# Kernel optimization log

Measured on AMD Instinct MI355X. Metric: run time of the kernel, lower is better.

Reference implementation:

```python
import jax, jax.numpy as jnp
import numpy as np

# 8 skeleton directions (unit step vectors (dy, dx)) at 45-degree increments.
# step idx selects the direction along which the 1D kernel taps are sampled.
DIRS = [(0, 1), (1, 1), (1, 0), (1, -1), (0, -1), (-1, -1), (-1, 0), (-1, 1)]
DILATION = 1


def setup_inputs() -> dict:
    key = jax.random.key(0)
    k1, k2 = jax.random.split(key)
    B, C, H, W = 16, 128, 112, 112
    O, K = 128, 3
    x = jax.random.normal(k1, (B, C, H, W), dtype=jnp.float32)
    # kaiming_uniform-like scale for relu: bound = sqrt(6 / fan_in), fan_in = C*K
    bound = float(np.sqrt(6.0 / (C * K)))
    weight = jax.random.uniform(k2, (O, C, K), dtype=jnp.float32, minval=-bound, maxval=bound)
    return {"x": x, "weight": weight}


def _skeleton_conv_all_dirs(x, weight, dilation):
    """Directional 1D conv with zero 'same' padding for each of 8 directions.

    x: [B,C,H,W], weight: [O,C,K] -> out: [B,O,8,H,W]
    out[b,o,d,h,w] = sum_{c,k} w[o,c,k] * x[b,c, h+(k-K//2)*dil*dy_d, w+(k-K//2)*dil*dx_d]
    (out-of-bounds samples treated as zero)
    """
    B, C, H, W = x.shape
    O, _, K = weight.shape
    center = K // 2
    pad = center * dilation
    xp = jnp.pad(x, ((0, 0), (0, 0), (pad, pad), (pad, pad)))
    outs = []
    for dy, dx in DIRS:
        # gather the K taps along this direction: [K, B, C, H, W]
        taps = jnp.stack(
            [
                xp[
                    :,
                    :,
                    pad + (k - center) * dilation * dy : pad + (k - center) * dilation * dy + H,
                    pad + (k - center) * dilation * dx : pad + (k - center) * dilation * dx + W,
                ]
                for k in range(K)
            ],
            axis=0,
        )
        outs.append(jnp.einsum("kbchw,ock->bohw", taps, weight))
    return jnp.stack(outs, axis=2)  # [B, O, 8, H, W]


def reference(x, weight):
    # norm=None, activation=None -> raw stacked directional conv outputs
    return _skeleton_conv_all_dirs(x, weight, DILATION)
```

## Files before the change

kernel.cpp:

```cpp
#include <hip/hip_runtime.h>


#define Bn 16
#define Cn 128
#define On 128
#define Hn 112
#define Wn 112
#define HW 12544
#define PBLK 128
#define LDP 130

typedef short short8 __attribute__((ext_vector_type(8)));
typedef float floatx4 __attribute__((ext_vector_type(4)));

__device__ __forceinline__ unsigned short f2bf(float f) {
    unsigned u = __float_as_uint(f);
    u += 0x7FFFu + ((u >> 16) & 1u);
    return (unsigned short)(u >> 16);
}
__device__ __forceinline__ float bf2f(unsigned short h) {
    return __uint_as_float(((unsigned)h) << 16);
}

__global__ __launch_bounds__(256) void prep_w(const float* __restrict__ w,
                                              unsigned short* __restrict__ wb) {
    int i = blockIdx.x * 256 + threadIdx.x;
    int k = i >> 14;
    int r = i & 16383;
    int o = r >> 7, c = r & 127;
    wb[i] = f2bf(w[(o * Cn + c) * 3 + k]);
}

__global__ __launch_bounds__(256) void k1_gemm(const float* __restrict__ x,
                                               const unsigned short* __restrict__ wb,
                                               unsigned short* __restrict__ yws,
                                               int b0, int yB) {
    __shared__ unsigned short xs[Cn * LDP];
    const int t = threadIdx.x;
    const int wv = t >> 6, lane = t & 63;
    const int n16 = lane & 15, q = lane >> 4;
    const int bl = blockIdx.y;
    const int b = b0 + bl;
    const int pb = blockIdx.x * PBLK;

    {
        const float4* xg = (const float4*)x;
        size_t xbase = (size_t)(b * Cn) * (HW / 4) + (size_t)blockIdx.x * (PBLK / 4);
        #pragma unroll
        for (int i = 0; i < 16; ++i) {
            int idx = i * 256 + t;
            int c = idx >> 5, p4 = (idx & 31) * 4;
            float4 v = xg[xbase + (size_t)c * (HW / 4) + (idx & 31)];
            int la = c * LDP + p4;
            xs[la + 0] = f2bf(v.x); xs[la + 1] = f2bf(v.y);
            xs[la + 2] = f2bf(v.z); xs[la + 3] = f2bf(v.w);
        }
    }

    short8 af[3][2][4];
    #pragma unroll
    for (int kk = 0; kk < 3; ++kk)
        #pragma unroll
        for (int oi = 0; oi < 2; ++oi) {
            int o = wv * 32 + oi * 16 + n16;
            #pragma unroll
            for (int kc = 0; kc < 4; ++kc)
                af[kk][oi][kc] = *(const short8*)(wb + ((kk * On + o) * Cn + kc * 32 + q * 8));
        }
    __syncthreads();

    for (int nt = 0; nt < PBLK / 16; ++nt) {
        int p0 = nt * 16;
        short8 bf[4];
        #pragma unroll
        for (int kc = 0; kc < 4; ++kc) {
            int cb = kc * 32 + q * 8;
            short8 v;
            #pragma unroll
            for (int j = 0; j < 8; ++j) v[j] = (short)xs[(cb + j) * LDP + p0 + n16];
            bf[kc] = v;
        }
        #pragma unroll
        for (int kk = 0; kk < 3; ++kk)
            #pragma unroll
            for (int oi = 0; oi < 2; ++oi) {
                floatx4 acc = {0.f, 0.f, 0.f, 0.f};
                #pragma unroll
                for (int kc = 0; kc < 4; ++kc)
                    acc = __builtin_amdgcn_mfma_f32_16x16x32_bf16(af[kk][oi][kc], bf[kc], acc, 0, 0, 0);
                #pragma unroll
                for (int r = 0; r < 4; ++r) {
                    int orow = wv * 32 + oi * 16 + q * 4 + r;
                    yws[((size_t)(kk * yB + bl) * On + orow) * HW + pb + p0 + n16] = f2bf(acc[r]);
                }
            }
    }
}

#define LROW 128
__global__ __launch_bounds__(448) void k2_combine(const unsigned short* __restrict__ yws,
                                                  float* __restrict__ out,
                                                  int b0, int yB) {
    __shared__ unsigned short yt[3 * 34 * LROW];
    const int t = threadIdx.x;
    const int ht = blockIdx.x;
    const int o = blockIdx.y;
    const int bl = blockIdx.z;
    const int b = b0 + bl;
    const int h0 = ht * 32;

    for (int i = t; i < 3 * 34 * 15; i += 448) {
        int rj = i / 15, seg = i - rj * 15;
        int k = rj / 34, hr = rj - k * 34;
        int h = h0 - 1 + hr;
        if (seg < 14) {
            short8 v = {0, 0, 0, 0, 0, 0, 0, 0};
            if (h >= 0 && h < Hn)
                v = *(const short8*)(yws + ((size_t)(k * yB + bl) * On + o) * HW + h * Wn + seg * 8);
            *(short8*)(yt + (k * 34 + hr) * LROW + 8 + seg * 8) = v;
        } else {
            yt[(k * 34 + hr) * LROW + 7] = 0;
            yt[(k * 34 + hr) * LROW + 120] = 0;
        }
    }
    __syncthreads();

    int hr = t / 14, g = t - hr * 14;
    int h = h0 + hr;
    if (h >= Hn) return;
    int lr = hr + 1;
    int jb = 8 + g * 8;

    float y0[3][10], y2[3][10], y1[8];
    #pragma unroll
    for (int r = 0; r < 3; ++r)
        #pragma unroll
        for (int j = 0; j < 10; ++j) {
            y0[r][j] = bf2f(yt[(0 * 34 + lr - 1 + r) * LROW + jb - 1 + j]);
            y2[r][j] = bf2f(yt[(2 * 34 + lr - 1 + r) * LROW + jb - 1 + j]);
        }
    #pragma unroll
    for (int j = 0; j < 8; ++j) y1[j] = bf2f(yt[(1 * 34 + lr) * LROW + jb + j]);

    const int DY[8] = {0, 1, 1, 1, 0, -1, -1, -1};
    const int DX[8] = {1, 1, 0, -1, -1, -1, 0, 1};
    size_t obase = ((size_t)(b * On + o) * 8) * HW + (size_t)h * Wn + g * 8;
    #pragma unroll
    for (int d = 0; d < 8; ++d) {
        int dy = DY[d], dx = DX[d];
        float vv[8];
        #pragma unroll
        for (int i = 0; i < 8; ++i)
            vv[i] = y1[i] + y0[1 - dy][i + 1 - dx] + y2[1 + dy][i + 1 + dx];
        float4* po = (float4*)(out + obase + (size_t)d * HW);
        po[0] = make_float4(vv[0], vv[1], vv[2], vv[3]);
        po[1] = make_float4(vv[4], vv[5], vv[6], vv[7]);
    }
}

__global__ __launch_bounds__(256) void k_naive(const float* __restrict__ x,
                                               const float* __restrict__ w,
                                               float* __restrict__ out) {
    const int DY[8] = {0, 1, 1, 1, 0, -1, -1, -1};
    const int DX[8] = {1, 1, 0, -1, -1, -1, 0, 1};
    size_t idx = (size_t)blockIdx.x * 256 + threadIdx.x;
    if (idx >= (size_t)Bn * On * 8 * HW) return;
    int ww = idx % Wn; size_t r = idx / Wn;
    int hh = r % Hn; r /= Hn;
    int d = r % 8; r /= 8;
    int o = r % On; int b = (int)(r / On);
    float s = 0.f;
    for (int c = 0; c < Cn; ++c)
        for (int k = 0; k < 3; ++k) {
            int h2 = hh + (k - 1) * DY[d], w2 = ww + (k - 1) * DX[d];
            if (h2 >= 0 && h2 < Hn && w2 >= 0 && w2 < Wn)
                s += w[(o * Cn + c) * 3 + k] * x[(size_t)(b * Cn + c) * HW + h2 * Wn + w2];
        }
    out[idx] = s;
}

extern "C" void kernel_launch(void* const* d_in, const int* in_sizes, int n_in,
                              void* d_out, int out_size, void* d_ws, size_t ws_size,
                              hipStream_t stream) {
    const float* x = (const float*)d_in[0];
    const float* w = (const float*)d_in[1];
    float* out = (float*)d_out;

    unsigned short* wb = (unsigned short*)d_ws;
    unsigned short* yws = (unsigned short*)((char*)d_ws + 98304);
    const size_t perB = (size_t)3 * On * HW * 2;
    size_t avail = ws_size > 98304 ? ws_size - 98304 : 0;
    int nb = (int)(avail / perB);
    if (nb > Bn) nb = Bn;

    if (nb < 1) {
        size_t total = (size_t)Bn * On * 8 * HW;
        k_naive<<<dim3((unsigned)((total + 255) / 256)), 256, 0, stream>>>(x, w, out);
        return;
    }

    prep_w<<<192, 256, 0, stream>>>(w, wb);
    for (int b0 = 0; b0 < Bn; b0 += nb) {
        int cnb = (Bn - b0 < nb) ? (Bn - b0) : nb;
        k1_gemm<<<dim3(HW / PBLK, cnb), 256, 0, stream>>>(x, wb, yws, b0, nb);
        k2_combine<<<dim3(4, On, cnb), 448, 0, stream>>>(yws, out, b0, nb);
    }
}
```

Before: 1.083 ms.

## Fuse GEMM and directional combine into one kernel computing all eight directions

Replaces the two-kernel pipeline, which wrote three per-tap bf16 intermediates to workspace and recombined them, with one kernel. Each block loads a halo tile of x into XOR-swizzled LDS and runs the MFMAs for each direction's shifted taps directly, pairing opposite directions so they share loaded fragments. Removes the intermediate round-trip through global memory and the second launch. In exchange it does more MFMA work, since the per-direction side taps are recomputed instead of shared, and it writes fp32 output as scattered scalar stores.

```diff
diff --git a/kernel.cpp b/kernel.cpp
--- a/kernel.cpp
+++ b/kernel.cpp
@@ -7,8 +7,9 @@
 #define Hn 112
 #define Wn 112
 #define HW 12544
-#define PBLK 128
-#define LDP 130
+
+#define NR 66
+#define LROW 128
 
 typedef short short8 __attribute__((ext_vector_type(8)));
 typedef float floatx4 __attribute__((ext_vector_type(4)));
@@ -17,9 +18,6 @@
     unsigned u = __float_as_uint(f);
     u += 0x7FFFu + ((u >> 16) & 1u);
     return (unsigned short)(u >> 16);
-}
-__device__ __forceinline__ float bf2f(unsigned short h) {
-    return __uint_as_float(((unsigned)h) << 16);
 }
 
 __global__ __launch_bounds__(256) void prep_w(const float* __restrict__ w,
@@ -31,130 +29,116 @@
     wb[i] = f2bf(w[(o * Cn + c) * 3 + k]);
 }
 
-__global__ __launch_bounds__(256) void k1_gemm(const float* __restrict__ x,
-                                               const unsigned short* __restrict__ wb,
-                                               unsigned short* __restrict__ yws,
-                                               int b0, int yB) {
-    __shared__ unsigned short xs[Cn * LDP];
+__global__ __launch_bounds__(256, 2) void conv8(const float* __restrict__ x,
+                                                const unsigned short* __restrict__ wb,
+                                                float* __restrict__ out) {
+    __shared__ unsigned short xs[4 * NR * LROW];
     const int t = threadIdx.x;
     const int wv = t >> 6, lane = t & 63;
     const int n16 = lane & 15, q = lane >> 4;
-    const int bl = blockIdx.y;
-    const int b = b0 + bl;
-    const int pb = blockIdx.x * PBLK;
+    const int bx = blockIdx.x;
+    const int b = blockIdx.y;
+    const int wc = bx & 1, hs = bx >> 1;
+    const int h0 = hs * 2;
+    const int wbase = wc * 64;
+    const int NT = wc ? 3 : 4;
 
     {
-        const float4* xg = (const float4*)x;
-        size_t xbase = (size_t)(b * Cn) * (HW / 4) + (size_t)blockIdx.x * (PBLK / 4);
-        #pragma unroll
-        for (int i = 0; i < 16; ++i) {
-            int idx = i * 256 + t;
-            int c = idx >> 5, p4 = (idx & 31) * 4;
-            float4 v = xg[xbase + (size_t)c * (HW / 4) + (idx & 31)];
-            int la = c * LDP + p4;
-            xs[la + 0] = f2bf(v.x); xs[la + 1] = f2bf(v.y);
-            xs[la + 2] = f2bf(v.z); xs[la + 3] = f2bf(v.w);
-        }
+        int4* p = (int4*)xs;
+        for (int i = t; i < (4 * NR * LROW) / 8; i += 256)
+            p[i] = make_int4(0, 0, 0, 0);
     }
 
     short8 af[3][2][4];
+    const int og = wv * 32;
     #pragma unroll
-    for (int kk = 0; kk < 3; ++kk)
+    for (int k = 0; k < 3; ++k)
         #pragma unroll
         for (int oi = 0; oi < 2; ++oi) {
-            int o = wv * 32 + oi * 16 + n16;
+            int o = og + oi * 16 + n16;
             #pragma unroll
             for (int kc = 0; kc < 4; ++kc)
-                af[kk][oi][kc] = *(const short8*)(wb + ((kk * On + o) * Cn + kc * 32 + q * 8));
+                af[k][oi][kc] = *(const short8*)(wb + ((k * On + o) * Cn + kc * 32 + q * 8));
         }
     __syncthreads();
 
-    for (int nt = 0; nt < PBLK / 16; ++nt) {
-        int p0 = nt * 16;
-        short8 bf[4];
+    for (int i = t; i < 4 * 128 * 18; i += 256) {
+        int slot = i % 18;
+        int rem = i / 18;
+        int c = rem & 127, hr = rem >> 7;
+        int h = h0 - 1 + hr;
+        if ((unsigned)h >= Hn) continue;
+        int w0 = wbase - 4 + slot * 4;
+        if (w0 < 0 || w0 >= Wn) continue;
+        float4 v = *(const float4*)(x + ((size_t)(b * Cn + c) * Hn + h) * Wn + w0);
+        float vv[4] = {v.x, v.y, v.z, v.w};
+        int wf0 = w0 - wbase + 1;
         #pragma unroll
-        for (int kc = 0; kc < 4; ++kc) {
-            int cb = kc * 32 + q * 8;
-            short8 v;
-            #pragma unroll
-            for (int j = 0; j < 8; ++j) v[j] = (short)xs[(cb + j) * LDP + p0 + n16];
-            bf[kc] = v;
-        }
-        #pragma unroll
-        for (int kk = 0; kk < 3; ++kk)
-            #pragma unroll
-            for (int oi = 0; oi < 2; ++oi) {
-                floatx4 acc = {0.f, 0.f, 0.f, 0.f};
-                #pragma unroll
-                for (int kc = 0; kc < 4; ++kc)
-                    acc = __builtin_amdgcn_mfma_f32_16x16x32_bf16(af[kk][oi][kc], bf[kc], acc, 0, 0, 0);
-                #pragma unroll
-                for (int r = 0; r < 4; ++r) {
-                    int orow = wv * 32 + oi * 16 + q * 4 + r;
-                    yws[((size_t)(kk * yB + bl) * On + orow) * HW + pb + p0 + n16] = f2bf(acc[r]);
-                }
+        for (int cc = 0; cc < 4; ++cc) {
+            int wf = wf0 + cc;
+            if ((unsigned)wf < NR) {
+                int r = hr * NR + wf;
+                xs[r * LROW + (c ^ ((r & 15) << 3))] = f2bf(vv[cc]);
             }
-    }
-}
-
-#define LROW 128
-__global__ __launch_bounds__(448) void k2_combine(const unsigned short* __restrict__ yws,
-                                                  float* __restrict__ out,
-                                                  int b0, int yB) {
-    __shared__ unsigned short yt[3 * 34 * LROW];
-    const int t = threadIdx.x;
-    const int ht = blockIdx.x;
-    const int o = blockIdx.y;
-    const int bl = blockIdx.z;
-    const int b = b0 + bl;
-    const int h0 = ht * 32;
-
-    for (int i = t; i < 3 * 34 * 15; i += 448) {
-        int rj = i / 15, seg = i - rj * 15;
-        int k = rj / 34, hr = rj - k * 34;
-        int h = h0 - 1 + hr;
-        if (seg < 14) {
-            short8 v = {0, 0, 0, 0, 0, 0, 0, 0};
-            if (h >= 0 && h < Hn)
-                v = *(const short8*)(yws + ((size_t)(k * yB + bl) * On + o) * HW + h * Wn + seg * 8);
-            *(short8*)(yt + (k * 34 + hr) * LROW + 8 + seg * 8) = v;
-        } else {
-            yt[(k * 34 + hr) * LROW + 7] = 0;
-            yt[(k * 34 + hr) * LROW + 120] = 0;
         }
     }
     __syncthreads();
 
-    int hr = t / 14, g = t - hr * 14;
-    int h = h0 + hr;
-    if (h >= Hn) return;
-    int lr = hr + 1;
-    int jb = 8 + g * 8;
+    const int DY[4] = {0, 1, 1, 1};
+    const int DX[4] = {1, 1, 0, -1};
 
-    float y0[3][10], y2[3][10], y1[8];
-    #pragma unroll
-    for (int r = 0; r < 3; ++r)
-        #pragma unroll
-        for (int j = 0; j < 10; ++j) {
-            y0[r][j] = bf2f(yt[(0 * 34 + lr - 1 + r) * LROW + jb - 1 + j]);
-            y2[r][j] = bf2f(yt[(2 * 34 + lr - 1 + r) * LROW + jb - 1 + j]);
+    for (int ht = 0; ht < 2; ++ht) {
+        const int h = h0 + ht;
+        for (int wt = 0; wt < NT; ++wt) {
+            const int rb = (1 + ht) * NR + 1 + wt * 16 + n16;
+            short8 fc[4];
+            #pragma unroll
+            for (int kc = 0; kc < 4; ++kc) {
+                int cb = kc * 32 + q * 8;
+                fc[kc] = *(const short8*)(xs + rb * LROW + (cb ^ ((rb & 15) << 3)));
+            }
+            floatx4 acc1[2];
+            #pragma unroll
+            for (int oi = 0; oi < 2; ++oi) {
+                floatx4 a = {0.f, 0.f, 0.f, 0.f};
+                #pragma unroll
+                for (int kc = 0; kc < 4; ++kc)
+                    a = __builtin_amdgcn_mfma_f32_16x16x32_bf16(af[1][oi][kc], fc[kc], a, 0, 0, 0);
+                acc1[oi] = a;
+            }
+            size_t obase = ((size_t)b * On * 8) * HW + (size_t)h * Wn + wbase + wt * 16 + n16;
+            #pragma unroll
+            for (int pr = 0; pr < 4; ++pr) {
+                int dy = DY[pr], dx = DX[pr];
+                int rm = rb - dy * NR - dx;
+                int rp = rb + dy * NR + dx;
+                short8 fm[4], fp[4];
+                #pragma unroll
+                for (int kc = 0; kc < 4; ++kc) {
+                    int cb = kc * 32 + q * 8;
+                    fm[kc] = *(const short8*)(xs + rm * LROW + (cb ^ ((rm & 15) << 3)));
+                    fp[kc] = *(const short8*)(xs + rp * LROW + (cb ^ ((rp & 15) << 3)));
+                }
+                #pragma unroll
+                for (int oi = 0; oi < 2; ++oi) {
+                    floatx4 ad = {0.f, 0.f, 0.f, 0.f};
+                    floatx4 ad4 = {0.f, 0.f, 0.f, 0.f};
+                    #pragma unroll
+                    for (int kc = 0; kc < 4; ++kc) {
+                        ad  = __builtin_amdgcn_mfma_f32_16x16x32_bf16(af[0][oi][kc], fm[kc], ad, 0, 0, 0);
+                        ad  = __builtin_amdgcn_mfma_f32_16x16x32_bf16(af[2][oi][kc], fp[kc], ad, 0, 0, 0);
+                        ad4 = __builtin_amdgcn_mfma_f32_16x16x32_bf16(af[0][oi][kc], fp[kc], ad4, 0, 0, 0);
+                        ad4 = __builtin_amdgcn_mfma_f32_16x16x32_bf16(af[2][oi][kc], fm[kc], ad4, 0, 0, 0);
+                    }
+                    #pragma unroll
+                    for (int rr = 0; rr < 4; ++rr) {
+                        int o = og + oi * 16 + q * 4 + rr;
+                        out[obase + ((size_t)o * 8 + pr) * HW]     = ad[rr]  + acc1[oi][rr];
+                        out[obase + ((size_t)o * 8 + pr + 4) * HW] = ad4[rr] + acc1[oi][rr];
+                    }
+                }
+            }
         }
-    #pragma unroll
-    for (int j = 0; j < 8; ++j) y1[j] = bf2f(yt[(1 * 34 + lr) * LROW + jb + j]);
-
-    const int DY[8] = {0, 1, 1, 1, 0, -1, -1, -1};
-    const int DX[8] = {1, 1, 0, -1, -1, -1, 0, 1};
-    size_t obase = ((size_t)(b * On + o) * 8) * HW + (size_t)h * Wn + g * 8;
-    #pragma unroll
-    for (int d = 0; d < 8; ++d) {
-        int dy = DY[d], dx = DX[d];
-        float vv[8];
-        #pragma unroll
-        for (int i = 0; i < 8; ++i)
-            vv[i] = y1[i] + y0[1 - dy][i + 1 - dx] + y2[1 + dy][i + 1 + dx];
-        float4* po = (float4*)(out + obase + (size_t)d * HW);
-        po[0] = make_float4(vv[0], vv[1], vv[2], vv[3]);
-        po[1] = make_float4(vv[4], vv[5], vv[6], vv[7]);
     }
 }
 
@@ -186,23 +170,13 @@
     const float* w = (const float*)d_in[1];
     float* out = (float*)d_out;
 
-    unsigned short* wb = (unsigned short*)d_ws;
-    unsigned short* yws = (unsigned short*)((char*)d_ws + 98304);
-    const size_t perB = (size_t)3 * On * HW * 2;
-    size_t avail = ws_size > 98304 ? ws_size - 98304 : 0;
-    int nb = (int)(avail / perB);
-    if (nb > Bn) nb = Bn;
-
-    if (nb < 1) {
+    if (ws_size < 98304) {
         size_t total = (size_t)Bn * On * 8 * HW;
         k_naive<<<dim3((unsigned)((total + 255) / 256)), 256, 0, stream>>>(x, w, out);
         return;
     }
 
+    unsigned short* wb = (unsigned short*)d_ws;
     prep_w<<<192, 256, 0, stream>>>(w, wb);
-    for (int b0 = 0; b0 < Bn; b0 += nb) {
-        int cnb = (Bn - b0 < nb) ? (Bn - b0) : nb;
-        k1_gemm<<<dim3(HW / PBLK, cnb), 256, 0, stream>>>(x, wb, yws, b0, nb);
-        k2_combine<<<dim3(4, On, cnb), 448, 0, stream>>>(yws, out, b0, nb);
-    }
+    conv8<<<dim3(112, Bn), 256, 0, stream>>>(x, wb, out);
 }
```

Result: no change. 1.081 ms (-0.1%).
